# Optimization experiments

Measured on AMD Instinct MI355X. Metric: run time of the kernel, lower is better.

## Reference

```python
import jax, jax.numpy as jnp
import numpy as np

B, S, D, H, T = 16, 512, 512, 8, 8
DK = D // H
SCALE = float(1.0 / np.sqrt(DK))
EPS = 1e-5


def setup_inputs() -> dict:
    key = jax.random.key(0)
    ks = jax.random.split(key, 12)
    s = float(1.0 / np.sqrt(D))  # torch Linear default init scale
    u = lambda k, shp: jax.random.uniform(k, shp, jnp.float32, -s, s)
    return {
        "x": jax.random.normal(ks[0], (B, S, D), jnp.float32),
        "x_type": jax.random.randint(ks[1], (B, S), 0, T, jnp.int32),
        "mask": jax.random.randint(ks[2], (B, S, S), 0, 2, jnp.int32),
        "Wq": u(ks[3], (T, D, D)), "bq": u(ks[4], (T, D)),
        "Wk": u(ks[5], (T, D, D)), "bk": u(ks[6], (T, D)),
        "Wv": u(ks[7], (T, D, D)), "bv": u(ks[8], (T, D)),
        "Wa": u(ks[9], (T, D, D)), "ba": u(ks[10], (T, D)),
        "gamma": jnp.ones((T, D), jnp.float32),
        "beta": jnp.zeros((T, D), jnp.float32),
    }


def _typed_proj(xf, t, W, b):
    # per-node-type linear 'experts': compute all T projections, select by type id
    # xf: [N, D], W: [T, D, D], b: [T, D], t: [N] -> [N, D]
    all_p = jnp.einsum('nd,tdh->nth', xf, W) + b[None]  # [N, T, D]
    return jnp.take_along_axis(all_p, t[:, None, None], axis=1)[:, 0]


def reference(x, x_type, mask, Wq, bq, Wk, bk, Wv, bv, Wa, ba, gamma, beta):
    xf = x.reshape(-1, D)          # [N, D], N = B*S
    t = x_type.reshape(-1)         # [N]

    # heterogeneous Q/K/V dispatch
    q = _typed_proj(xf, t, Wq, bq).reshape(B, S, H, DK).transpose(0, 2, 1, 3)
    k = _typed_proj(xf, t, Wk, bk).reshape(B, S, H, DK).transpose(0, 2, 1, 3)
    v = _typed_proj(xf, t, Wv, bv).reshape(B, S, H, DK).transpose(0, 2, 1, 3)

    # scaled dot-product attention with boolean mask (mask==0 -> -1e9)
    scores = jnp.einsum('bhqd,bhkd->bhqk', q, k) * SCALE  # [B, H, S, S]
    scores = jnp.where(mask[:, None] == 0, jnp.float32(-1e9), scores)
    p = jax.nn.softmax(scores, axis=-1)
    att = jnp.einsum('bhqk,bhkd->bhqd', p, v)             # [B, H, S, DK]
    att = att.transpose(0, 2, 1, 3).reshape(-1, D)        # [N, D]

    # per-type output projection + residual + per-type LayerNorm
    a = _typed_proj(att, t, Wa, ba)
    h = a + xf
    mu = jnp.mean(h, axis=-1, keepdims=True)
    var = jnp.mean((h - mu) ** 2, axis=-1, keepdims=True)
    out = (h - mu) * jax.lax.rsqrt(var + EPS) * gamma[t] + beta[t]
    return out.reshape(B, S, D)
```

## Files before the change

kernel.cpp:

```cpp
#include <hip/hip_runtime.h>
#include <hip/hip_bf16.h>

typedef __attribute__((ext_vector_type(8))) short short8;
typedef __attribute__((ext_vector_type(4))) float f32x4;
typedef __attribute__((ext_vector_type(4))) unsigned short u16x4;
typedef unsigned short u16;
typedef unsigned long long u64;

#define NB 16
#define NS 512
#define ND 512
#define NH 8
#define NT 8
#define NDK 64
#define NN (NB*NS)
#define SCALE_LOG2E 0.18033688011112042f
#define BM 128
#define BN 128
#define BKK 64

__device__ __forceinline__ u16 f2bf(float f) {
    __hip_bfloat16 h = __float2bfloat16(f);
    return *reinterpret_cast<u16*>(&h);
}

typedef const __attribute__((address_space(1))) void* gas_t;
typedef __attribute__((address_space(3))) void* las_t;

__device__ __forceinline__ void gload16(const void* gsrc, void* ldst) {
    __builtin_amdgcn_global_load_lds((gas_t)gsrc, (las_t)ldst, 16, 0, 0);
}

__global__ __launch_bounds__(256) void bucketize(
    const int* __restrict__ xty, int* __restrict__ perm, int* __restrict__ typeoff,
    int* __restrict__ tile_type, int* __restrict__ tile_row0, int* __restrict__ ntiles)
{
    __shared__ int cnt[NT], off[NT + 1], cur[NT];
    int tid = threadIdx.x;
    if (tid < NT) cnt[tid] = 0;
    __syncthreads();
    for (int n = tid; n < NN; n += 256) atomicAdd(&cnt[xty[n]], 1);
    __syncthreads();
    if (tid == 0) {
        int acc = 0, nt = 0;
        for (int t = 0; t < NT; ++t) {
            off[t] = acc;
            for (int r = 0; r < cnt[t]; r += BM) { tile_type[nt] = t; tile_row0[nt] = acc + r; ++nt; }
            acc += cnt[t];
        }
        off[NT] = acc;
        *ntiles = nt;
        for (int t = 0; t <= NT; ++t) typeoff[t] = off[t];
    }
    __syncthreads();
    if (tid < NT) cur[tid] = off[tid];
    __syncthreads();
    for (int n = tid; n < NN; n += 256) {
        int t = xty[n];
        int p = atomicAdd(&cur[t], 1);
        perm[p] = n;
    }
}

__global__ __launch_bounds__(256) void cvt_x(const float* __restrict__ x, u16* __restrict__ xb)
{
    int i = blockIdx.x * 256 + threadIdx.x;
    float4 v = reinterpret_cast<const float4*>(x)[i];
    u16x4 o;
    o.x = f2bf(v.x); o.y = f2bf(v.y); o.z = f2bf(v.z); o.w = f2bf(v.w);
    reinterpret_cast<u16x4*>(xb)[i] = o;
}

__global__ __launch_bounds__(256) void cvt_w(
    const float* __restrict__ Wq, const float* __restrict__ Wk,
    const float* __restrict__ Wv, const float* __restrict__ Wa,
    u16* __restrict__ Wqt, u16* __restrict__ Wkt, u16* __restrict__ Wvt, u16* __restrict__ Wat)
{
    int arr = blockIdx.z >> 3, t = blockIdx.z & 7;
    const float* W = (arr == 0 ? Wq : arr == 1 ? Wk : arr == 2 ? Wv : Wa) + ((size_t)t << 18);
    u16* O = (arr == 0 ? Wqt : arr == 1 ? Wkt : arr == 2 ? Wvt : Wat) + ((size_t)t << 18);
    int d0 = blockIdx.x * 64, h0 = blockIdx.y * 64;
    __shared__ __align__(16) float tile[64][68];
    int tx = threadIdx.x & 15, ty = threadIdx.x >> 4;
    #pragma unroll
    for (int i = 0; i < 4; ++i) {
        int r = ty + i * 16;
        float4 v = *reinterpret_cast<const float4*>(&W[(size_t)(d0 + r) * ND + h0 + tx * 4]);
        *reinterpret_cast<float4*>(&tile[r][tx * 4]) = v;
    }
    __syncthreads();
    #pragma unroll
    for (int i = 0; i < 4; ++i) {
        int r = ty + i * 16;
        u16x4 o;
        o.x = f2bf(tile[tx * 4 + 0][r]);
        o.y = f2bf(tile[tx * 4 + 1][r]);
        o.z = f2bf(tile[tx * 4 + 2][r]);
        o.w = f2bf(tile[tx * 4 + 3][r]);
        *reinterpret_cast<u16x4*>(&O[(size_t)(h0 + r) * ND + d0 + tx * 4]) = o;
    }
}

__global__ __launch_bounds__(256) void pack_mask(const int* __restrict__ mask, u64* __restrict__ maskb)
{
    int i = blockIdx.x * 256 + threadIdx.x;
    int v = mask[i];
    u64 bal = __ballot(v != 0);
    if ((threadIdx.x & 63) == 0) maskb[i >> 6] = bal;
}

__global__ __launch_bounds__(256) void qkv_gemm(
    const u16* __restrict__ xb,
    const u16* __restrict__ Wqt, const u16* __restrict__ Wkt, const u16* __restrict__ Wvt,
    const float* __restrict__ bq, const float* __restrict__ bk, const float* __restrict__ bv,
    const int* __restrict__ perm, const int* __restrict__ typeoff,
    const int* __restrict__ tile_type, const int* __restrict__ tile_row0, const int* __restrict__ ntiles,
    u16* __restrict__ qb, u16* __restrict__ kbf, u16* __restrict__ vb)
{
    if (blockIdx.x >= *ntiles) return;
    int t = tile_type[blockIdx.x];
    int row0 = tile_row0[blockIdx.x];
    int rows = typeoff[t + 1] - row0; if (rows > BM) rows = BM;
    int proj = blockIdx.y >> 2;
    int col0 = (blockIdx.y & 3) * BN;
    const u16* W = (proj == 0 ? Wqt : proj == 1 ? Wkt : Wvt) + ((size_t)t << 18);
    const float* bias = (proj == 0 ? bq : proj == 1 ? bk : bv) + (t << 9);
    u16* outp = proj == 0 ? qb : proj == 1 ? kbf : vb;
    float qscale = proj == 0 ? SCALE_LOG2E : 1.f;

    __shared__ __align__(16) u16 As[BM][BKK];
    __shared__ __align__(16) u16 Bs[BN][BKK];
    __shared__ int stok[BM];

    int tid = threadIdx.x;
    if (tid < BM) stok[tid] = perm[row0 + (tid < rows ? tid : 0)];
    __syncthreads();

    int lane = tid & 63, w = tid >> 6;
    int wr = w >> 1, wc = w & 1;
    int fr = lane & 15, g = lane >> 4;

    int lrow = lane >> 3;
    int schunk = (lane & 7) ^ lrow;
    int tokA[4];
    #pragma unroll
    for (int k = 0; k < 4; ++k) tokA[k] = stok[w * 32 + k * 8 + lrow];

    f32x4 acc[4][4] = {};

    for (int k0 = 0; k0 < ND; k0 += BKK) {
        __syncthreads();
        #pragma unroll
        for (int k = 0; k < 4; ++k) {
            gload16(xb + (((size_t)tokA[k]) << 9) + k0 + schunk * 8, &As[w * 32 + k * 8][0]);
            gload16(W + (((size_t)(col0 + w * 32 + k * 8 + lrow)) << 9) + k0 + schunk * 8,
                    &Bs[w * 32 + k * 8][0]);
        }
        __syncthreads();

        const char* Ab = (const char*)As;
        const char* Bb = (const char*)Bs;
        #pragma unroll
        for (int ks = 0; ks < 2; ++ks) {
            short8 af[4], bfr[4];
            #pragma unroll
            for (int m = 0; m < 4; ++m) {
                int r = wr * 64 + m * 16 + fr;
                af[m] = *reinterpret_cast<const short8*>(Ab + r * 128 + (((ks * 4 + g) ^ (r & 7)) << 4));
            }
            #pragma unroll
            for (int n = 0; n < 4; ++n) {
                int r = wc * 64 + n * 16 + fr;
                bfr[n] = *reinterpret_cast<const short8*>(Bb + r * 128 + (((ks * 4 + g) ^ (r & 7)) << 4));
            }
            #pragma unroll
            for (int m = 0; m < 4; ++m)
                #pragma unroll
                for (int n = 0; n < 4; ++n)
                    acc[m][n] = __builtin_amdgcn_mfma_f32_16x16x32_bf16(af[m], bfr[n], acc[m][n], 0, 0, 0);
        }
    }

    int rbase = g << 2;
    #pragma unroll
    for (int n = 0; n < 4; ++n) {
        int c = col0 + wc * 64 + n * 16 + fr;
        float bv_ = bias[c];
        int h = c >> 6, dk = c & 63;
        #pragma unroll
        for (int m = 0; m < 4; ++m) {
            #pragma unroll
            for (int i = 0; i < 4; ++i) {
                int r = wr * 64 + m * 16 + rbase + i;
                if (r < rows) {
                    int tok = stok[r];
                    int b = tok >> 9, s = tok & 511;
                    outp[((size_t)((b * NH + h) * NS + s) << 6) + dk] =
                        f2bf((acc[m][n][i] + bv_) * qscale);
                }
            }
        }
    }
}

__global__ __launch_bounds__(256) void transp_v(const u16* __restrict__ vb, u16* __restrict__ vtb)
{
    int bh = blockIdx.y, s0 = blockIdx.x * 64;
    __shared__ __align__(16) u16 t[64][72];
    int tid = threadIdx.x;
    const u16* src = vb + ((size_t)bh << 15) + ((size_t)s0 << 6);
    #pragma unroll
    for (int it = 0; it < 2; ++it) {
        int idx = it * 256 + tid;
        int s = idx & 63, c = idx >> 6;
        short8 v = *reinterpret_cast<const short8*>(src + ((size_t)s << 6) + c * 8);
        #pragma unroll
        for (int j = 0; j < 8; ++j) t[c * 8 + j][s] = ((const u16*)&v)[j];
    }
    __syncthreads();
    u16* dst = vtb + ((size_t)bh << 15) + s0;
    #pragma unroll
    for (int it = 0; it < 2; ++it) {
        int idx = it * 256 + tid;
        int dk = idx >> 3, c = idx & 7;
        short8 v = *reinterpret_cast<const short8*>(&t[dk][c * 8]);
        *reinterpret_cast<short8*>(dst + (size_t)dk * NS + c * 8) = v;
    }
}

__global__ __launch_bounds__(256) void attn_mfma(
    const u16* __restrict__ qb, const u16* __restrict__ kbf, const u16* __restrict__ vtb,
    const u64* __restrict__ maskb, u16* __restrict__ attb)
{
    int bh = blockIdx.y;
    int b = bh >> 3, h = bh & 7;
    int q0 = blockIdx.x * 64;
    int tid = threadIdx.x, lane = tid & 63, w = tid >> 6;
    int ln15 = lane & 15, g = lane >> 4;

    __shared__ __align__(16) u16 sK[64 * 64];
    __shared__ __align__(16) u16 sVt[64 * 64];
    __shared__ __align__(16) u16 sP[4 * 16 * 72];

    const u16* Qg = qb + ((size_t)(bh * NS + q0 + w * 16 + ln15) << 6);
    short8 aq0 = *reinterpret_cast<const short8*>(Qg + g * 8);
    short8 aq1 = *reinterpret_cast<const short8*>(Qg + 32 + g * 8);

    const u16* Kg = kbf + ((size_t)bh << 15);
    const u16* Vtg = vtb + ((size_t)bh << 15);
    int srow = tid >> 3, schunk = tid & 7;

    const u64* Mrow = maskb + (size_t)((b << 9) + q0 + w * 16 + g * 4) * 8;

    f32x4 acc_o[4] = {};
    float mrun[4], lrun[4];
    #pragma unroll
    for (int i = 0; i < 4; ++i) { mrun[i] = -3.0e38f; lrun[i] = 0.f; }

    short8 kpre0 = *reinterpret_cast<const short8*>(Kg + ((size_t)srow << 6) + schunk * 8);
    short8 kpre1 = *reinterpret_cast<const short8*>(Kg + ((size_t)(srow + 32) << 6) + schunk * 8);
    short8 vpre0 = *reinterpret_cast<const short8*>(Vtg + (size_t)srow * NS + schunk * 8);
    short8 vpre1 = *reinterpret_cast<const short8*>(Vtg + (size_t)(srow + 32) * NS + schunk * 8);

    u16* sPw = sP + w * 16 * 72;

    for (int j = 0; j < 8; ++j) {
        __syncthreads();
        {
            int r2 = srow + 32;
            *reinterpret_cast<short8*>((char*)sK  + srow * 128 + ((schunk * 16) ^ ((srow & 7) << 4))) = kpre0;
            *reinterpret_cast<short8*>((char*)sK  + r2   * 128 + ((schunk * 16) ^ ((r2   & 7) << 4))) = kpre1;
            *reinterpret_cast<short8*>((char*)sVt + srow * 128 + ((schunk * 16) ^ ((srow & 7) << 4))) = vpre0;
            *reinterpret_cast<short8*>((char*)sVt + r2   * 128 + ((schunk * 16) ^ ((r2   & 7) << 4))) = vpre1;
        }
        if (j < 7) {
            int j1 = j + 1;
            kpre0 = *reinterpret_cast<const short8*>(Kg + ((size_t)(j1 * 64 + srow) << 6) + schunk * 8);
            kpre1 = *reinterpret_cast<const short8*>(Kg + ((size_t)(j1 * 64 + srow + 32) << 6) + schunk * 8);
            vpre0 = *reinterpret_cast<const short8*>(Vtg + (size_t)srow * NS + j1 * 64 + schunk * 8);
            vpre1 = *reinterpret_cast<const short8*>(Vtg + (size_t)(srow + 32) * NS + j1 * 64 + schunk * 8);
        }
        __syncthreads();

        f32x4 accs[4] = {};
        #pragma unroll
        for (int ks = 0; ks < 2; ++ks) {
            short8 a = ks ? aq1 : aq0;
            #pragma unroll
            for (int n = 0; n < 4; ++n) {
                int row = n * 16 + ln15;
                short8 bk = *reinterpret_cast<const short8*>(
                    (char*)sK + row * 128 + (((ks * 64) + g * 16) ^ ((row & 7) << 4)));
                accs[n] = __builtin_amdgcn_mfma_f32_16x16x32_bf16(a, bk, accs[n], 0, 0, 0);
            }
        }

        #pragma unroll
        for (int i = 0; i < 4; ++i) {
            u64 mw = Mrow[(size_t)i * 8 + j];
            float sv[4];
            #pragma unroll
            for (int n = 0; n < 4; ++n)
                sv[n] = ((mw >> (n * 16 + ln15)) & 1ull) ? accs[n][i] : -1.0e9f;
            float mx = fmaxf(fmaxf(sv[0], sv[1]), fmaxf(sv[2], sv[3]));
            #pragma unroll
            for (int d = 1; d < 16; d <<= 1) mx = fmaxf(mx, __shfl_xor(mx, d));
            float nm = fmaxf(mrun[i], mx);
            float sc = exp2f(mrun[i] - nm);
            float ps = 0.f;
            #pragma unroll
            for (int n = 0; n < 4; ++n) {
                float p = exp2f(sv[n] - nm);
                ps += p;
                sPw[(g * 4 + i) * 72 + n * 16 + ln15] = f2bf(p);
            }
            mrun[i] = nm;
            lrun[i] = lrun[i] * sc + ps;
            #pragma unroll
            for (int n2 = 0; n2 < 4; ++n2) acc_o[n2][i] *= sc;
        }

        #pragma unroll
        for (int ks = 0; ks < 2; ++ks) {
            short8 ap = *reinterpret_cast<const short8*>(
                (char*)sPw + ((ln15 * 72 + ks * 32 + g * 8) << 1));
            #pragma unroll
            for (int n2 = 0; n2 < 4; ++n2) {
                int row = n2 * 16 + ln15;
                short8 bv = *reinterpret_cast<const short8*>(
                    (char*)sVt + row * 128 + (((ks * 64) + g * 16) ^ ((row & 7) << 4)));
                acc_o[n2] = __builtin_amdgcn_mfma_f32_16x16x32_bf16(ap, bv, acc_o[n2], 0, 0, 0);
            }
        }
    }

    float linv[4];
    #pragma unroll
    for (int i = 0; i < 4; ++i) {
        float l = lrun[i];
        #pragma unroll
        for (int d = 1; d < 16; d <<= 1) l += __shfl_xor(l, d);
        linv[i] = 1.f / l;
    }
    #pragma unroll
    for (int n2 = 0; n2 < 4; ++n2) {
        #pragma unroll
        for (int i = 0; i < 4; ++i) {
            int q = q0 + w * 16 + g * 4 + i;
            attb[((size_t)((b << 9) + q) << 9) + (h << 6) + n2 * 16 + ln15] =
                f2bf(acc_o[n2][i] * linv[i]);
        }
    }
}

__global__ __launch_bounds__(256) void out_gemm(
    const u16* __restrict__ attb, const u16* __restrict__ Wat, const float* __restrict__ ba,
    const int* __restrict__ perm, const int* __restrict__ typeoff,
    const int* __restrict__ tile_type, const int* __restrict__ tile_row0, const int* __restrict__ ntiles,
    const float* __restrict__ x, float* __restrict__ hbuf)
{
    if (blockIdx.x >= *ntiles) return;
    int t = tile_type[blockIdx.x];
    int row0 = tile_row0[blockIdx.x];
    int rows = typeoff[t + 1] - row0; if (rows > BM) rows = BM;
    int col0 = blockIdx.y * BN;
    const u16* W = Wat + ((size_t)t << 18);
    const float* bias = ba + (t << 9);

    __shared__ __align__(16) u16 As[BM][BKK];
    __shared__ __align__(16) u16 Bs[BN][BKK];
    __shared__ int stok[BM];

    int tid = threadIdx.x;
    if (tid < BM) stok[tid] = perm[row0 + (tid < rows ? tid : 0)];
    __syncthreads();

    int lane = tid & 63, w = tid >> 6;
    int wr = w >> 1, wc = w & 1;
    int fr = lane & 15, g = lane >> 4;

    int lrow = lane >> 3;
    int schunk = (lane & 7) ^ lrow;
    int tokA[4];
    #pragma unroll
    for (int k = 0; k < 4; ++k) tokA[k] = stok[w * 32 + k * 8 + lrow];

    f32x4 acc[4][4] = {};

    for (int k0 = 0; k0 < ND; k0 += BKK) {
        __syncthreads();
        #pragma unroll
        for (int k = 0; k < 4; ++k) {
            gload16(attb + (((size_t)tokA[k]) << 9) + k0 + schunk * 8, &As[w * 32 + k * 8][0]);
            gload16(W + (((size_t)(col0 + w * 32 + k * 8 + lrow)) << 9) + k0 + schunk * 8,
                    &Bs[w * 32 + k * 8][0]);
        }
        __syncthreads();

        const char* Ab = (const char*)As;
        const char* Bb = (const char*)Bs;
        #pragma unroll
        for (int ks = 0; ks < 2; ++ks) {
            short8 af[4], bfr[4];
            #pragma unroll
            for (int m = 0; m < 4; ++m) {
                int r = wr * 64 + m * 16 + fr;
                af[m] = *reinterpret_cast<const short8*>(Ab + r * 128 + (((ks * 4 + g) ^ (r & 7)) << 4));
            }
            #pragma unroll
            for (int n = 0; n < 4; ++n) {
                int r = wc * 64 + n * 16 + fr;
                bfr[n] = *reinterpret_cast<const short8*>(Bb + r * 128 + (((ks * 4 + g) ^ (r & 7)) << 4));
            }
            #pragma unroll
            for (int m = 0; m < 4; ++m)
                #pragma unroll
                for (int n = 0; n < 4; ++n)
                    acc[m][n] = __builtin_amdgcn_mfma_f32_16x16x32_bf16(af[m], bfr[n], acc[m][n], 0, 0, 0);
        }
    }

    int rbase = g << 2;
    #pragma unroll
    for (int n = 0; n < 4; ++n) {
        int c = col0 + wc * 64 + n * 16 + fr;
        float bv_ = bias[c];
        #pragma unroll
        for (int m = 0; m < 4; ++m) {
            #pragma unroll
            for (int i = 0; i < 4; ++i) {
                int r = wr * 64 + m * 16 + rbase + i;
                if (r < rows) {
                    int tok = stok[r];
                    size_t off = (size_t)tok * ND + c;
                    hbuf[off] = acc[m][n][i] + bv_ + x[off];
                }
            }
        }
    }
}

__global__ __launch_bounds__(256) void lnorm(
    const float* __restrict__ hbuf, const int* __restrict__ xty,
    const float* __restrict__ gamma, const float* __restrict__ beta, float* __restrict__ out)
{
    int row = blockIdx.x * 4 + (threadIdx.x >> 6);
    int lane = threadIdx.x & 63;
    const float4* h4 = reinterpret_cast<const float4*>(hbuf + (size_t)row * ND);
    float4 a = h4[lane * 2], b = h4[lane * 2 + 1];
    float sum = a.x + a.y + a.z + a.w + b.x + b.y + b.z + b.w;
    float sq = a.x * a.x + a.y * a.y + a.z * a.z + a.w * a.w
             + b.x * b.x + b.y * b.y + b.z * b.z + b.w * b.w;
    #pragma unroll
    for (int off = 32; off; off >>= 1) { sum += __shfl_xor(sum, off); sq += __shfl_xor(sq, off); }
    float mu = sum * (1.f / ND);
    float var = sq * (1.f / ND) - mu * mu;
    float is = rsqrtf(var + 1e-5f);
    int t = xty[row];
    const float4* g4 = reinterpret_cast<const float4*>(gamma + ((size_t)t << 9));
    const float4* be4 = reinterpret_cast<const float4*>(beta + ((size_t)t << 9));
    float4 g0 = g4[lane * 2], g1 = g4[lane * 2 + 1];
    float4 b0 = be4[lane * 2], b1 = be4[lane * 2 + 1];
    float4 o0, o1;
    o0.x = (a.x - mu) * is * g0.x + b0.x;
    o0.y = (a.y - mu) * is * g0.y + b0.y;
    o0.z = (a.z - mu) * is * g0.z + b0.z;
    o0.w = (a.w - mu) * is * g0.w + b0.w;
    o1.x = (b.x - mu) * is * g1.x + b1.x;
    o1.y = (b.y - mu) * is * g1.y + b1.y;
    o1.z = (b.z - mu) * is * g1.z + b1.z;
    o1.w = (b.w - mu) * is * g1.w + b1.w;
    float4* out4 = reinterpret_cast<float4*>(out + (size_t)row * ND);
    out4[lane * 2] = o0; out4[lane * 2 + 1] = o1;
}

extern "C" void kernel_launch(void* const* d_in, const int* in_sizes, int n_in,
                              void* d_out, int out_size, void* d_ws, size_t ws_size,
                              hipStream_t stream)
{
    const float* x     = (const float*)d_in[0];
    const int*   xty   = (const int*)d_in[1];
    const int*   mask  = (const int*)d_in[2];
    const float* Wq    = (const float*)d_in[3];
    const float* bq    = (const float*)d_in[4];
    const float* Wk    = (const float*)d_in[5];
    const float* bk    = (const float*)d_in[6];
    const float* Wv    = (const float*)d_in[7];
    const float* bv    = (const float*)d_in[8];
    const float* Wa    = (const float*)d_in[9];
    const float* ba    = (const float*)d_in[10];
    const float* gamma = (const float*)d_in[11];
    const float* beta  = (const float*)d_in[12];
    float* out = (float*)d_out;

    char* ws = (char*)d_ws;
    u16*   xb      = (u16*)(ws + 0);
    u16*   Wqt     = (u16*)(ws + 8388608);
    u16*   Wkt     = (u16*)(ws + 12582912);
    u16*   Wvt     = (u16*)(ws + 16777216);
    u16*   Wat     = (u16*)(ws + 20971520);
    u16*   qb      = (u16*)(ws + 25165824);
    u16*   kbf     = (u16*)(ws + 33554432);
    u16*   vb      = (u16*)(ws + 41943040);
    u16*   vtb     = (u16*)(ws + 50331648);
    u16*   attb    = (u16*)(ws + 58720256);
    float* hbuf    = (float*)(ws + 67108864);
    u64*   maskb   = (u64*)(ws + 83886080);
    int*   perm    = (int*)(ws + 84410368);
    int*   typeoff = (int*)(ws + 84443136);
    int*   ttile   = (int*)(ws + 84443200);
    int*   trow    = (int*)(ws + 84443520);
    int*   ntiles  = (int*)(ws + 84443840);

    bucketize<<<dim3(1), dim3(256), 0, stream>>>(xty, perm, typeoff, ttile, trow, ntiles);
    cvt_x<<<dim3(4096), dim3(256), 0, stream>>>(x, xb);
    cvt_w<<<dim3(8, 8, 32), dim3(256), 0, stream>>>(Wq, Wk, Wv, Wa, Wqt, Wkt, Wvt, Wat);
    pack_mask<<<dim3(16384), dim3(256), 0, stream>>>(mask, maskb);
    qkv_gemm<<<dim3(72, 12), dim3(256), 0, stream>>>(xb, Wqt, Wkt, Wvt, bq, bk, bv,
                                                     perm, typeoff, ttile, trow, ntiles, qb, kbf, vb);
    transp_v<<<dim3(8, 128), dim3(256), 0, stream>>>(vb, vtb);
    attn_mfma<<<dim3(8, 128), dim3(256), 0, stream>>>(qb, kbf, vtb, maskb, attb);
    out_gemm<<<dim3(72, 4), dim3(256), 0, stream>>>(attb, Wat, ba,
                                                    perm, typeoff, ttile, trow, ntiles, x, hbuf);
    lnorm<<<dim3(2048), dim3(256), 0, stream>>>(hbuf, xty, gamma, beta, out);
}
```

Before: 279.3 us.

## Double-buffer GEMM loads, remap blocks for XCD locality, restructure attention softmax

The typed QKV and output GEMMs now double-buffer the LDS tiles, issuing the next K-slice's global-to-LDS loads before computing the current one. This overlaps memory latency with MFMA work. All three main kernels use a 1D grid with a block-index remap that spreads work across the 8 XCDs so neighbouring tiles and heads share cache. The attention kernel swaps the MFMA operand order so each lane owns one query row, which cuts the cross-lane max and sum reductions. It also skips the accumulator rescale unless the running max grows by more than a threshold, and writes P as packed bf16 pairs into a narrower LDS stride. The lazy rescale relies on the bounded exponent for accuracy, and double buffering doubles the GEMM LDS footprint.

```diff
diff --git a/kernel.cpp b/kernel.cpp
--- a/kernel.cpp
+++ b/kernel.cpp
@@ -5,6 +5,7 @@
 typedef __attribute__((ext_vector_type(4))) float f32x4;
 typedef __attribute__((ext_vector_type(4))) unsigned short u16x4;
 typedef unsigned short u16;
+typedef unsigned int u32;
 typedef unsigned long long u64;
 
 #define NB 16
@@ -23,6 +24,9 @@
     __hip_bfloat16 h = __float2bfloat16(f);
     return *reinterpret_cast<u16*>(&h);
 }
+__device__ __forceinline__ u32 pk2(float lo, float hi) {
+    return (u32)f2bf(lo) | ((u32)f2bf(hi) << 16);
+}
 
 typedef const __attribute__((address_space(1))) void* gas_t;
 typedef __attribute__((address_space(3))) void* las_t;
@@ -117,19 +121,21 @@
     const int* __restrict__ tile_type, const int* __restrict__ tile_row0, const int* __restrict__ ntiles,
     u16* __restrict__ qb, u16* __restrict__ kbf, u16* __restrict__ vb)
 {
-    if (blockIdx.x >= *ntiles) return;
-    int t = tile_type[blockIdx.x];
-    int row0 = tile_row0[blockIdx.x];
+    int work = (blockIdx.x & 7) * 108 + (blockIdx.x >> 3);
+    int tile = work / 12, pc = work % 12;
+    if (tile >= *ntiles) return;
+    int t = tile_type[tile];
+    int row0 = tile_row0[tile];
     int rows = typeoff[t + 1] - row0; if (rows > BM) rows = BM;
-    int proj = blockIdx.y >> 2;
-    int col0 = (blockIdx.y & 3) * BN;
+    int proj = pc >> 2;
+    int col0 = (pc & 3) * BN;
     const u16* W = (proj == 0 ? Wqt : proj == 1 ? Wkt : Wvt) + ((size_t)t << 18);
     const float* bias = (proj == 0 ? bq : proj == 1 ? bk : bv) + (t << 9);
     u16* outp = proj == 0 ? qb : proj == 1 ? kbf : vb;
     float qscale = proj == 0 ? SCALE_LOG2E : 1.f;
 
-    __shared__ __align__(16) u16 As[BM][BKK];
-    __shared__ __align__(16) u16 Bs[BN][BKK];
+    __shared__ __align__(16) u16 As[2][BM][BKK];
+    __shared__ __align__(16) u16 Bs[2][BM][BKK];
     __shared__ int stok[BM];
 
     int tid = threadIdx.x;
@@ -146,20 +152,31 @@
     #pragma unroll
     for (int k = 0; k < 4; ++k) tokA[k] = stok[w * 32 + k * 8 + lrow];
 
+    auto stage = [&](int buf, int k0) {
+        #pragma unroll
+        for (int k = 0; k < 4; ++k) {
+            gload16(xb + (((size_t)tokA[k]) << 9) + k0 + schunk * 8, &As[buf][w * 32 + k * 8][0]);
+            gload16(W + (((size_t)(col0 + w * 32 + k * 8 + lrow)) << 9) + k0 + schunk * 8,
+                    &Bs[buf][w * 32 + k * 8][0]);
+        }
+    };
+
     f32x4 acc[4][4] = {};
 
-    for (int k0 = 0; k0 < ND; k0 += BKK) {
-        __syncthreads();
-        #pragma unroll
-        for (int k = 0; k < 4; ++k) {
-            gload16(xb + (((size_t)tokA[k]) << 9) + k0 + schunk * 8, &As[w * 32 + k * 8][0]);
-            gload16(W + (((size_t)(col0 + w * 32 + k * 8 + lrow)) << 9) + k0 + schunk * 8,
-                    &Bs[w * 32 + k * 8][0]);
-        }
-        __syncthreads();
-
-        const char* Ab = (const char*)As;
-        const char* Bb = (const char*)Bs;
+    stage(0, 0);
+    #pragma unroll
+    for (int it = 0; it < 8; ++it) {
+        int cur = it & 1;
+        if (it < 7) {
+            stage(cur ^ 1, (it + 1) * BKK);
+            asm volatile("s_waitcnt vmcnt(8)" ::: "memory");
+        } else {
+            asm volatile("s_waitcnt vmcnt(0)" ::: "memory");
+        }
+        __builtin_amdgcn_s_barrier();
+
+        const char* Ab = (const char*)As[cur];
+        const char* Bb = (const char*)Bs[cur];
         #pragma unroll
         for (int ks = 0; ks < 2; ++ks) {
             short8 af[4], bfr[4];
@@ -179,6 +196,8 @@
                 for (int n = 0; n < 4; ++n)
                     acc[m][n] = __builtin_amdgcn_mfma_f32_16x16x32_bf16(af[m], bfr[n], acc[m][n], 0, 0, 0);
         }
+        asm volatile("s_waitcnt lgkmcnt(0)" ::: "memory");
+        __builtin_amdgcn_s_barrier();
     }
 
     int rbase = g << 2;
@@ -232,15 +251,16 @@
     const u16* __restrict__ qb, const u16* __restrict__ kbf, const u16* __restrict__ vtb,
     const u64* __restrict__ maskb, u16* __restrict__ attb)
 {
-    int bh = blockIdx.y;
+    int work = (blockIdx.x & 7) * 128 + (blockIdx.x >> 3);
+    int bh = work >> 3, jq = work & 7;
     int b = bh >> 3, h = bh & 7;
-    int q0 = blockIdx.x * 64;
+    int q0 = jq * 64;
     int tid = threadIdx.x, lane = tid & 63, w = tid >> 6;
     int ln15 = lane & 15, g = lane >> 4;
 
     __shared__ __align__(16) u16 sK[64 * 64];
     __shared__ __align__(16) u16 sVt[64 * 64];
-    __shared__ __align__(16) u16 sP[4 * 16 * 72];
+    __shared__ __align__(16) u16 sP[4 * 16 * 68];
 
     const u16* Qg = qb + ((size_t)(bh * NS + q0 + w * 16 + ln15) << 6);
     short8 aq0 = *reinterpret_cast<const short8*>(Qg + g * 8);
@@ -250,19 +270,16 @@
     const u16* Vtg = vtb + ((size_t)bh << 15);
     int srow = tid >> 3, schunk = tid & 7;
 
-    const u64* Mrow = maskb + (size_t)((b << 9) + q0 + w * 16 + g * 4) * 8;
-
+    const u64* Mq = maskb + ((size_t)((b << 9) + q0 + w * 16 + ln15)) * 8;
+    float mrun = -3.0e38f, lrun = 0.f;
     f32x4 acc_o[4] = {};
-    float mrun[4], lrun[4];
-    #pragma unroll
-    for (int i = 0; i < 4; ++i) { mrun[i] = -3.0e38f; lrun[i] = 0.f; }
 
     short8 kpre0 = *reinterpret_cast<const short8*>(Kg + ((size_t)srow << 6) + schunk * 8);
     short8 kpre1 = *reinterpret_cast<const short8*>(Kg + ((size_t)(srow + 32) << 6) + schunk * 8);
     short8 vpre0 = *reinterpret_cast<const short8*>(Vtg + (size_t)srow * NS + schunk * 8);
     short8 vpre1 = *reinterpret_cast<const short8*>(Vtg + (size_t)(srow + 32) * NS + schunk * 8);
 
-    u16* sPw = sP + w * 16 * 72;
+    char* sPw = (char*)sP + w * 16 * 136;
 
     for (int j = 0; j < 8; ++j) {
         __syncthreads();
@@ -285,70 +302,80 @@
         f32x4 accs[4] = {};
         #pragma unroll
         for (int ks = 0; ks < 2; ++ks) {
-            short8 a = ks ? aq1 : aq0;
+            short8 bq_ = ks ? aq1 : aq0;
             #pragma unroll
             for (int n = 0; n < 4; ++n) {
                 int row = n * 16 + ln15;
-                short8 bk = *reinterpret_cast<const short8*>(
+                short8 kfrag = *reinterpret_cast<const short8*>(
                     (char*)sK + row * 128 + (((ks * 64) + g * 16) ^ ((row & 7) << 4)));
-                accs[n] = __builtin_amdgcn_mfma_f32_16x16x32_bf16(a, bk, accs[n], 0, 0, 0);
-            }
-        }
-
-        #pragma unroll
-        for (int i = 0; i < 4; ++i) {
-            u64 mw = Mrow[(size_t)i * 8 + j];
-            float sv[4];
-            #pragma unroll
-            for (int n = 0; n < 4; ++n)
-                sv[n] = ((mw >> (n * 16 + ln15)) & 1ull) ? accs[n][i] : -1.0e9f;
-            float mx = fmaxf(fmaxf(sv[0], sv[1]), fmaxf(sv[2], sv[3]));
-            #pragma unroll
-            for (int d = 1; d < 16; d <<= 1) mx = fmaxf(mx, __shfl_xor(mx, d));
-            float nm = fmaxf(mrun[i], mx);
-            float sc = exp2f(mrun[i] - nm);
-            float ps = 0.f;
-            #pragma unroll
-            for (int n = 0; n < 4; ++n) {
-                float p = exp2f(sv[n] - nm);
-                ps += p;
-                sPw[(g * 4 + i) * 72 + n * 16 + ln15] = f2bf(p);
-            }
-            mrun[i] = nm;
-            lrun[i] = lrun[i] * sc + ps;
-            #pragma unroll
-            for (int n2 = 0; n2 < 4; ++n2) acc_o[n2][i] *= sc;
-        }
+                accs[n] = __builtin_amdgcn_mfma_f32_16x16x32_bf16(kfrag, bq_, accs[n], 0, 0, 0);
+            }
+        }
+
+        u64 mw = Mq[j];
+        float sv[4][4];
+        float mx = -3.0e38f;
+        #pragma unroll
+        for (int n = 0; n < 4; ++n) {
+            u32 b4 = (u32)(mw >> (n * 16 + g * 4)) & 15u;
+            #pragma unroll
+            for (int r = 0; r < 4; ++r) {
+                float s = (b4 >> r) & 1u ? accs[n][r] : -1.0e9f;
+                sv[n][r] = s;
+                mx = fmaxf(mx, s);
+            }
+        }
+        mx = fmaxf(mx, __shfl_xor(mx, 16));
+        mx = fmaxf(mx, __shfl_xor(mx, 32));
+
+        if (__any(mx > mrun + 8.f)) {
+            float nm = fmaxf(mrun, mx);
+            float sc = exp2f(mrun - nm);
+            mrun = nm;
+            lrun *= sc;
+            #pragma unroll
+            for (int i = 0; i < 4; ++i) {
+                float si = __shfl(sc, g * 4 + i);
+                #pragma unroll
+                for (int n2 = 0; n2 < 4; ++n2) acc_o[n2][i] *= si;
+            }
+        }
+
+        float ps = 0.f;
+        #pragma unroll
+        for (int n = 0; n < 4; ++n) {
+            float p0 = exp2f(sv[n][0] - mrun), p1 = exp2f(sv[n][1] - mrun);
+            float p2 = exp2f(sv[n][2] - mrun), p3 = exp2f(sv[n][3] - mrun);
+            ps += (p0 + p1) + (p2 + p3);
+            *reinterpret_cast<u32*>(sPw + ln15 * 136 + n * 32 + g * 8 + 0) = pk2(p0, p1);
+            *reinterpret_cast<u32*>(sPw + ln15 * 136 + n * 32 + g * 8 + 4) = pk2(p2, p3);
+        }
+        ps += __shfl_xor(ps, 16);
+        ps += __shfl_xor(ps, 32);
+        lrun += ps;
 
         #pragma unroll
         for (int ks = 0; ks < 2; ++ks) {
-            short8 ap = *reinterpret_cast<const short8*>(
-                (char*)sPw + ((ln15 * 72 + ks * 32 + g * 8) << 1));
+            short8 ap = *reinterpret_cast<const short8*>(sPw + ln15 * 136 + ks * 64 + g * 16);
             #pragma unroll
             for (int n2 = 0; n2 < 4; ++n2) {
                 int row = n2 * 16 + ln15;
-                short8 bv = *reinterpret_cast<const short8*>(
+                short8 vfrag = *reinterpret_cast<const short8*>(
                     (char*)sVt + row * 128 + (((ks * 64) + g * 16) ^ ((row & 7) << 4)));
-                acc_o[n2] = __builtin_amdgcn_mfma_f32_16x16x32_bf16(ap, bv, acc_o[n2], 0, 0, 0);
-            }
-        }
-    }
-
-    float linv[4];
+                acc_o[n2] = __builtin_amdgcn_mfma_f32_16x16x32_bf16(ap, vfrag, acc_o[n2], 0, 0, 0);
+            }
+        }
+    }
+
+    float linv = 1.f / lrun;
     #pragma unroll
     for (int i = 0; i < 4; ++i) {
-        float l = lrun[i];
-        #pragma unroll
-        for (int d = 1; d < 16; d <<= 1) l += __shfl_xor(l, d);
-        linv[i] = 1.f / l;
-    }
-    #pragma unroll
-    for (int n2 = 0; n2 < 4; ++n2) {
-        #pragma unroll
-        for (int i = 0; i < 4; ++i) {
-            int q = q0 + w * 16 + g * 4 + i;
+        float li = __shfl(linv, g * 4 + i);
+        int q = q0 + w * 16 + g * 4 + i;
+        #pragma unroll
+        for (int n2 = 0; n2 < 4; ++n2) {
             attb[((size_t)((b << 9) + q) << 9) + (h << 6) + n2 * 16 + ln15] =
-                f2bf(acc_o[n2][i] * linv[i]);
+                f2bf(acc_o[n2][i] * li);
         }
     }
 }
@@ -359,16 +386,18 @@
     const int* __restrict__ tile_type, const int* __restrict__ tile_row0, const int* __restrict__ ntiles,
     const float* __restrict__ x, float* __restrict__ hbuf)
 {
-    if (blockIdx.x >= *ntiles) return;
-    int t = tile_type[blockIdx.x];
-    int row0 = tile_row0[blockIdx.x];
+    int work = (blockIdx.x & 7) * 36 + (blockIdx.x >> 3);
+    int tile = work >> 2;
+    if (tile >= *ntiles) return;
+    int t = tile_type[tile];
+    int row0 = tile_row0[tile];
     int rows = typeoff[t + 1] - row0; if (rows > BM) rows = BM;
-    int col0 = blockIdx.y * BN;
+    int col0 = (work & 3) * BN;
     const u16* W = Wat + ((size_t)t << 18);
     const float* bias = ba + (t << 9);
 
-    __shared__ __align__(16) u16 As[BM][BKK];
-    __shared__ __align__(16) u16 Bs[BN][BKK];
+    __shared__ __align__(16) u16 As[2][BM][BKK];
+    __shared__ __align__(16) u16 Bs[2][BM][BKK];
     __shared__ int stok[BM];
 
     int tid = threadIdx.x;
@@ -385,20 +414,31 @@
     #pragma unroll
     for (int k = 0; k < 4; ++k) tokA[k] = stok[w * 32 + k * 8 + lrow];
 
+    auto stage = [&](int buf, int k0) {
+        #pragma unroll
+        for (int k = 0; k < 4; ++k) {
+            gload16(attb + (((size_t)tokA[k]) << 9) + k0 + schunk * 8, &As[buf][w * 32 + k * 8][0]);
+            gload16(W + (((size_t)(col0 + w * 32 + k * 8 + lrow)) << 9) + k0 + schunk * 8,
+                    &Bs[buf][w * 32 + k * 8][0]);
+        }
+    };
+
     f32x4 acc[4][4] = {};
 
-    for (int k0 = 0; k0 < ND; k0 += BKK) {
-        __syncthreads();
-        #pragma unroll
-        for (int k = 0; k < 4; ++k) {
-            gload16(attb + (((size_t)tokA[k]) << 9) + k0 + schunk * 8, &As[w * 32 + k * 8][0]);
-            gload16(W + (((size_t)(col0 + w * 32 + k * 8 + lrow)) << 9) + k0 + schunk * 8,
-                    &Bs[w * 32 + k * 8][0]);
-        }
-        __syncthreads();
-
-        const char* Ab = (const char*)As;
-        const char* Bb = (const char*)Bs;
+    stage(0, 0);
+    #pragma unroll
+    for (int it = 0; it < 8; ++it) {
+        int cur = it & 1;
+        if (it < 7) {
+            stage(cur ^ 1, (it + 1) * BKK);
+            asm volatile("s_waitcnt vmcnt(8)" ::: "memory");
+        } else {
+            asm volatile("s_waitcnt vmcnt(0)" ::: "memory");
+        }
+        __builtin_amdgcn_s_barrier();
+
+        const char* Ab = (const char*)As[cur];
+        const char* Bb = (const char*)Bs[cur];
         #pragma unroll
         for (int ks = 0; ks < 2; ++ks) {
             short8 af[4], bfr[4];
@@ -418,6 +458,8 @@
                 for (int n = 0; n < 4; ++n)
                     acc[m][n] = __builtin_amdgcn_mfma_f32_16x16x32_bf16(af[m], bfr[n], acc[m][n], 0, 0, 0);
         }
+        asm volatile("s_waitcnt lgkmcnt(0)" ::: "memory");
+        __builtin_amdgcn_s_barrier();
     }
 
     int rbase = g << 2;
@@ -516,11 +558,11 @@
     cvt_x<<<dim3(4096), dim3(256), 0, stream>>>(x, xb);
     cvt_w<<<dim3(8, 8, 32), dim3(256), 0, stream>>>(Wq, Wk, Wv, Wa, Wqt, Wkt, Wvt, Wat);
     pack_mask<<<dim3(16384), dim3(256), 0, stream>>>(mask, maskb);
-    qkv_gemm<<<dim3(72, 12), dim3(256), 0, stream>>>(xb, Wqt, Wkt, Wvt, bq, bk, bv,
-                                                     perm, typeoff, ttile, trow, ntiles, qb, kbf, vb);
+    qkv_gemm<<<dim3(864), dim3(256), 0, stream>>>(xb, Wqt, Wkt, Wvt, bq, bk, bv,
+                                                  perm, typeoff, ttile, trow, ntiles, qb, kbf, vb);
     transp_v<<<dim3(8, 128), dim3(256), 0, stream>>>(vb, vtb);
-    attn_mfma<<<dim3(8, 128), dim3(256), 0, stream>>>(qb, kbf, vtb, maskb, attb);
-    out_gemm<<<dim3(72, 4), dim3(256), 0, stream>>>(attb, Wat, ba,
-                                                    perm, typeoff, ttile, trow, ntiles, x, hbuf);
+    attn_mfma<<<dim3(1024), dim3(256), 0, stream>>>(qb, kbf, vtb, maskb, attb);
+    out_gemm<<<dim3(288), dim3(256), 0, stream>>>(attb, Wat, ba,
+                                                  perm, typeoff, ttile, trow, ntiles, x, hbuf);
     lnorm<<<dim3(2048), dim3(256), 0, stream>>>(hbuf, xty, gamma, beta, out);
 }
```

New measurement: 270.9 us. 3.0% less time.
